# Performance work log

Hardware: AMD Instinct MI355X
Metric: run time of the kernel (lower is better)

## Reference

```python
import jax, jax.numpy as jnp
import numpy as np

N = 100000          # number of nodes (src == dst in this sampled graph)
DEG = 8             # uniform sampled fan-in (max_num_neighbors)
E = N * DEG         # number of edges
IN_C = 128
HEADS = 4
OUT_C = 32
NEG_SLOPE = 0.2


def setup_inputs() -> dict:
    key = jax.random.key(0)
    k1, k2, k3, k4, k5 = jax.random.split(key, 5)
    x = jax.random.normal(k1, (N, IN_C), dtype=jnp.float32)
    csr_row_ptr = jnp.arange(N + 1, dtype=jnp.int64) * DEG
    csr_col_ind = jax.random.randint(k2, (E,), 0, N, dtype=jnp.int64)
    # learned params (xavier-normal-ish scaling)
    lin_w = jax.random.normal(k3, (IN_C, HEADS * OUT_C), dtype=jnp.float32) * np.sqrt(2.0 / (IN_C + HEADS * OUT_C))
    att = jax.random.normal(k4, (2 * HEADS * OUT_C,), dtype=jnp.float32) * np.sqrt(2.0 / (1 + OUT_C))
    bias = jnp.zeros((HEADS * OUT_C,), dtype=jnp.float32)
    return {"x": x, "csr_row_ptr": csr_row_ptr, "csr_col_ind": csr_col_ind,
            "max_num_neighbors": DEG, "lin_w": lin_w, "att": att, "bias": bias}


def reference(x, csr_row_ptr, csr_col_ind, max_num_neighbors, lin_w, att, bias):
    n = x.shape[0]
    e = csr_col_ind.shape[0]
    hc = HEADS * OUT_C
    # linear projection: [N, H, C]
    xp = (x @ lin_w).reshape(n, HEADS, OUT_C)
    att_src = att[:hc].reshape(HEADS, OUT_C)
    att_dst = att[hc:].reshape(HEADS, OUT_C)
    # per-node attention logits per head: [N, H]
    a_src = jnp.einsum('nhc,hc->nh', xp, att_src)
    a_dst = jnp.einsum('nhc,hc->nh', xp, att_dst)
    # expand CSR row_ptr into per-edge destination ids: [E]
    dst = jnp.searchsorted(csr_row_ptr, jnp.arange(e, dtype=csr_row_ptr.dtype), side='right') - 1
    src = csr_col_ind
    # edge scores + per-destination softmax over incoming edges
    logits = jax.nn.leaky_relu(a_src[src] + a_dst[dst], NEG_SLOPE)  # [E, H]
    m = jax.ops.segment_max(logits, dst, num_segments=n)            # [N, H]
    ex = jnp.exp(logits - m[dst])
    denom = jax.ops.segment_sum(ex, dst, num_segments=n)            # [N, H]
    alpha = ex / denom[dst]                                         # [E, H]
    # weighted aggregation of neighbor features: [N, H, C]
    out = jax.ops.segment_sum(alpha[:, :, None] * xp[src], dst, num_segments=n)
    out = out.reshape(n, hc) + bias  # concat=True
    return out
```

## Files before the change

kernel.cpp:

```cpp
#include <hip/hip_runtime.h>
#include <stdint.h>

#define HEADS 4
#define NEG_SLOPE 0.2f
#define NPB 4
#define MB 128

typedef _Float16 f16;
typedef f16 f16x8 __attribute__((ext_vector_type(8)));
typedef f16 f16x2 __attribute__((ext_vector_type(2)));
typedef float f32x4 __attribute__((ext_vector_type(4)));

#define SWZ(row, kb) (((row) << 8) + ((kb) ^ (((row) & 7) << 4)))

__global__ __launch_bounds__(256) void wt_kernel(const float* __restrict__ w,
                                                 f16* __restrict__ wt) {
    __shared__ f16 tl[16][136];
    const int b = blockIdx.x, t = threadIdx.x;
    for (int i = t; i < 2048; i += 256) {
        int k = i >> 4, nl = i & 15;
        tl[nl][k] = (f16)w[k * 128 + b * 16 + nl];
    }
    __syncthreads();
    {
        int nl = t >> 4, kc = t & 15;
        f16x8 v = *(const f16x8*)&tl[nl][kc * 8];
        *(f16x8*)(wt + (b * 16 + nl) * 128 + kc * 8) = v;
    }
}

__global__ __launch_bounds__(256) void gat_proj_mfma(
    const float* __restrict__ x, const f16* __restrict__ wt,
    const float* __restrict__ att, f16* __restrict__ xp,
    float* __restrict__ a_src, float* __restrict__ a_dst, int n) {
    __shared__ unsigned char lds[65536];
    __shared__ float att_l[256];
    const int t = threadIdx.x;
    const int node0 = blockIdx.x * MB;
    const int lane = t & 63;
    const int wv = t >> 6;

    att_l[t] = att[t];

    for (int i = t; i < 2048; i += 256) {
        int row = i >> 4, kc = i & 15;
        uint4 v = *(const uint4*)(wt + row * 128 + kc * 8);
        *(uint4*)(lds + SWZ(row, kc * 16)) = v;
    }
    for (int i = t; i < 2048; i += 256) {
        int row = i >> 4, kc = i & 15;
        int grow = node0 + row;
        float4 a = make_float4(0.f, 0.f, 0.f, 0.f), b = a;
        if (grow < n) {
            const float4* p = (const float4*)(x + (size_t)grow * 128 + kc * 8);
            a = p[0];
            b = p[1];
        }
        f16x8 hv;
        hv[0] = (f16)a.x; hv[1] = (f16)a.y; hv[2] = (f16)a.z; hv[3] = (f16)a.w;
        hv[4] = (f16)b.x; hv[5] = (f16)b.y; hv[6] = (f16)b.z; hv[7] = (f16)b.w;
        *(f16x8*)(lds + 32768 + SWZ(row, kc * 16)) = hv;
    }
    __syncthreads();

    f32x4 acc[2][8];
#pragma unroll
    for (int mi = 0; mi < 2; mi++)
#pragma unroll
        for (int nf = 0; nf < 8; nf++)
            acc[mi][nf] = (f32x4){0.f, 0.f, 0.f, 0.f};

#pragma unroll
    for (int kt = 0; kt < 4; kt++) {
        const int kb = kt * 64 + (lane >> 4) * 16;
        f16x8 afr[2];
#pragma unroll
        for (int mi = 0; mi < 2; mi++) {
            int row = wv * 32 + mi * 16 + (lane & 15);
            afr[mi] = *(const f16x8*)(lds + 32768 + SWZ(row, kb));
        }
#pragma unroll
        for (int nf = 0; nf < 8; nf++) {
            int wrow = nf * 16 + (lane & 15);
            f16x8 bfr = *(const f16x8*)(lds + SWZ(wrow, kb));
            acc[0][nf] = __builtin_amdgcn_mfma_f32_16x16x32_f16(afr[0], bfr, acc[0][nf], 0, 0, 0);
            acc[1][nf] = __builtin_amdgcn_mfma_f32_16x16x32_f16(afr[1], bfr, acc[1][nf], 0, 0, 0);
        }
    }

    __syncthreads();
#pragma unroll
    for (int mi = 0; mi < 2; mi++)
#pragma unroll
        for (int r = 0; r < 4; r++) {
            int row = wv * 32 + mi * 16 + (lane >> 4) * 4 + r;
#pragma unroll
            for (int nf = 0; nf < 8; nf++) {
                int col = nf * 16 + (lane & 15);
                *(f16*)(lds + 32768 + SWZ(row, col * 2)) = (f16)acc[mi][nf][r];
            }
        }
    __syncthreads();

    for (int i = t; i < MB * HEADS; i += 256) {
        int row = i >> 2, h = i & 3;
        int grow = node0 + row;
        if (grow < n) {
            float s = 0.f, d = 0.f;
#pragma unroll
            for (int cc = 0; cc < 4; cc++) {
                f16x8 v = *(const f16x8*)(lds + 32768 + SWZ(row, h * 64 + cc * 16));
#pragma unroll
                for (int j = 0; j < 8; j++) {
                    float xv = (float)v[j];
                    int c = cc * 8 + j;
                    s = fmaf(xv, att_l[h * 32 + c], s);
                    d = fmaf(xv, att_l[128 + h * 32 + c], d);
                }
            }
            a_src[(size_t)grow * HEADS + h] = s;
            a_dst[(size_t)grow * HEADS + h] = d;
        }
    }
    for (int i = t; i < 2048; i += 256) {
        int row = i >> 4, kc = i & 15;
        int grow = node0 + row;
        if (grow < n)
            *(uint4*)(xp + (size_t)grow * 128 + kc * 8) =
                *(const uint4*)(lds + 32768 + SWZ(row, kc * 16));
    }
}

__global__ __launch_bounds__(256) void gat_aggr_kernel(
    const f16* __restrict__ xp, const float* __restrict__ a_src,
    const float* __restrict__ a_dst, const int* __restrict__ row_ptr,
    const int* __restrict__ col_ind, const float* __restrict__ bias,
    float* __restrict__ out, int n) {
    __shared__ float alpha_l[NPB][32];
    __shared__ int src_l[NPB][8];
    const int t = threadIdx.x;
    const int w = t >> 6;
    const int lane = t & 63;
    const int node = blockIdx.x * NPB + w;

    int deg = 0;
    if (node < n) {
        int rs = row_ptr[node];
        int re = row_ptr[node + 1];
        deg = re - rs;
        if (deg > 8) deg = 8;
        if (lane < 8) src_l[w][lane] = (lane < deg) ? col_ind[rs + lane] : 0;
    }
    __syncthreads();

    if (node < n && lane < 32) {
        const int e = lane >> 2, h = lane & 3;
        float v = -1e30f;
        if (e < deg) {
            int s = src_l[w][e];
            float z = a_src[(size_t)s * HEADS + h] + a_dst[(size_t)node * HEADS + h];
            v = (z >= 0.f) ? z : NEG_SLOPE * z;
        }
        float m = v;
        m = fmaxf(m, __shfl_xor(m, 4, 64));
        m = fmaxf(m, __shfl_xor(m, 8, 64));
        m = fmaxf(m, __shfl_xor(m, 16, 64));
        float ex = (e < deg) ? __expf(v - m) : 0.f;
        float ssum = ex;
        ssum += __shfl_xor(ssum, 4, 64);
        ssum += __shfl_xor(ssum, 8, 64);
        ssum += __shfl_xor(ssum, 16, 64);
        alpha_l[w][lane] = ex / ssum;
    }
    __syncthreads();
    if (node >= n) return;

    const int c0 = lane * 2;
    const int h = lane >> 4;
    float acc0 = 0.f, acc1 = 0.f;
    if (deg == 8) {
        f16x2 pv[8];
#pragma unroll
        for (int e = 0; e < 8; e++)
            pv[e] = *(const f16x2*)(xp + (size_t)src_l[w][e] * 128 + c0);
#pragma unroll
        for (int e = 0; e < 8; e++) {
            float a = alpha_l[w][e * 4 + h];
            acc0 = fmaf(a, (float)pv[e][0], acc0);
            acc1 = fmaf(a, (float)pv[e][1], acc1);
        }
    } else {
        for (int e = 0; e < deg; e++) {
            float a = alpha_l[w][e * 4 + h];
            f16x2 pv = *(const f16x2*)(xp + (size_t)src_l[w][e] * 128 + c0);
            acc0 = fmaf(a, (float)pv[0], acc0);
            acc1 = fmaf(a, (float)pv[1], acc1);
        }
    }
    float2 b2 = ((const float2*)bias)[lane];
    ((float2*)(out + (size_t)node * 128))[lane] = make_float2(acc0 + b2.x, acc1 + b2.y);
}

extern "C" void kernel_launch(void* const* d_in, const int* in_sizes, int n_in,
                              void* d_out, int out_size, void* d_ws, size_t ws_size,
                              hipStream_t stream) {
    const float* x = (const float*)d_in[0];
    const int* row_ptr = (const int*)d_in[1];
    const int* col_ind = (const int*)d_in[2];
    const float* lin_w = (const float*)d_in[4];
    const float* att = (const float*)d_in[5];
    const float* bias = (const float*)d_in[6];
    float* out = (float*)d_out;
    const int n = in_sizes[0] / 128;

    f16* xp = (f16*)d_ws;
    float* a_src = (float*)((char*)d_ws + (size_t)n * 128 * 2);
    float* a_dst = a_src + (size_t)n * HEADS;
    f16* wt = (f16*)(a_dst + (size_t)n * HEADS);

    hipLaunchKernelGGL(wt_kernel, dim3(8), dim3(256), 0, stream, lin_w, wt);
    hipLaunchKernelGGL(gat_proj_mfma, dim3((n + MB - 1) / MB), dim3(256), 0, stream,
                       x, wt, att, xp, a_src, a_dst, n);
    hipLaunchKernelGGL(gat_aggr_kernel, dim3((n + NPB - 1) / NPB), dim3(256), 0, stream,
                       xp, a_src, a_dst, row_ptr, col_ind, bias, out, n);
}
```

Before: 81.60 us.

## Shrink projection tile to 64 rows and make aggregation shared-memory-free

The projection kernel now handles 64 nodes per block with one 16-row MFMA tile per wave, which cuts LDS use and doubles the grid to raise occupancy. The aggregation kernel drops shared memory and block barriers. Source ids are broadcast with wave shuffles, the feature gathers are issued before the softmax so their latency is hidden, and each half-wave loads 8-byte f16x4 chunks for 4 edges before the halves are combined with a xor-shuffle. A zero-sum guard is added to the normalisation. The trade-off is extra shuffle work and idle upper lanes during the final store.

```diff
diff --git a/kernel.cpp b/kernel.cpp
--- a/kernel.cpp
+++ b/kernel.cpp
@@ -3,12 +3,11 @@
 
 #define HEADS 4
 #define NEG_SLOPE 0.2f
-#define NPB 4
-#define MB 128
+#define MB 64
 
 typedef _Float16 f16;
 typedef f16 f16x8 __attribute__((ext_vector_type(8)));
-typedef f16 f16x2 __attribute__((ext_vector_type(2)));
+typedef f16 f16x4 __attribute__((ext_vector_type(4)));
 typedef float f32x4 __attribute__((ext_vector_type(4)));
 
 #define SWZ(row, kb) (((row) << 8) + ((kb) ^ (((row) & 7) << 4)))
@@ -33,7 +32,7 @@
     const float* __restrict__ x, const f16* __restrict__ wt,
     const float* __restrict__ att, f16* __restrict__ xp,
     float* __restrict__ a_src, float* __restrict__ a_dst, int n) {
-    __shared__ unsigned char lds[65536];
+    __shared__ unsigned char lds[49152];
     __shared__ float att_l[256];
     const int t = threadIdx.x;
     const int node0 = blockIdx.x * MB;
@@ -47,7 +46,7 @@
         uint4 v = *(const uint4*)(wt + row * 128 + kc * 8);
         *(uint4*)(lds + SWZ(row, kc * 16)) = v;
     }
-    for (int i = t; i < 2048; i += 256) {
+    for (int i = t; i < 1024; i += 256) {
         int row = i >> 4, kc = i & 15;
         int grow = node0 + row;
         float4 a = make_float4(0.f, 0.f, 0.f, 0.f), b = a;
@@ -63,47 +62,37 @@
     }
     __syncthreads();
 
-    f32x4 acc[2][8];
-#pragma unroll
-    for (int mi = 0; mi < 2; mi++)
-#pragma unroll
-        for (int nf = 0; nf < 8; nf++)
-            acc[mi][nf] = (f32x4){0.f, 0.f, 0.f, 0.f};
+    f32x4 acc[8];
+#pragma unroll
+    for (int nf = 0; nf < 8; nf++) acc[nf] = (f32x4){0.f, 0.f, 0.f, 0.f};
 
 #pragma unroll
     for (int kt = 0; kt < 4; kt++) {
         const int kb = kt * 64 + (lane >> 4) * 16;
-        f16x8 afr[2];
-#pragma unroll
-        for (int mi = 0; mi < 2; mi++) {
-            int row = wv * 32 + mi * 16 + (lane & 15);
-            afr[mi] = *(const f16x8*)(lds + 32768 + SWZ(row, kb));
-        }
+        int arow = wv * 16 + (lane & 15);
+        f16x8 afr = *(const f16x8*)(lds + 32768 + SWZ(arow, kb));
 #pragma unroll
         for (int nf = 0; nf < 8; nf++) {
             int wrow = nf * 16 + (lane & 15);
             f16x8 bfr = *(const f16x8*)(lds + SWZ(wrow, kb));
-            acc[0][nf] = __builtin_amdgcn_mfma_f32_16x16x32_f16(afr[0], bfr, acc[0][nf], 0, 0, 0);
-            acc[1][nf] = __builtin_amdgcn_mfma_f32_16x16x32_f16(afr[1], bfr, acc[1][nf], 0, 0, 0);
-        }
-    }
-
-    __syncthreads();
-#pragma unroll
-    for (int mi = 0; mi < 2; mi++)
-#pragma unroll
-        for (int r = 0; r < 4; r++) {
-            int row = wv * 32 + mi * 16 + (lane >> 4) * 4 + r;
-#pragma unroll
-            for (int nf = 0; nf < 8; nf++) {
-                int col = nf * 16 + (lane & 15);
-                *(f16*)(lds + 32768 + SWZ(row, col * 2)) = (f16)acc[mi][nf][r];
-            }
-        }
-    __syncthreads();
-
-    for (int i = t; i < MB * HEADS; i += 256) {
-        int row = i >> 2, h = i & 3;
+            acc[nf] = __builtin_amdgcn_mfma_f32_16x16x32_f16(afr, bfr, acc[nf], 0, 0, 0);
+        }
+    }
+
+    __syncthreads();
+#pragma unroll
+    for (int r = 0; r < 4; r++) {
+        int row = wv * 16 + (lane >> 4) * 4 + r;
+#pragma unroll
+        for (int nf = 0; nf < 8; nf++) {
+            int col = nf * 16 + (lane & 15);
+            *(f16*)(lds + 32768 + SWZ(row, col * 2)) = (f16)acc[nf][r];
+        }
+    }
+    __syncthreads();
+
+    {
+        int row = t >> 2, h = t & 3;
         int grow = node0 + row;
         if (grow < n) {
             float s = 0.f, d = 0.f;
@@ -122,7 +111,7 @@
             a_dst[(size_t)grow * HEADS + h] = d;
         }
     }
-    for (int i = t; i < 2048; i += 256) {
+    for (int i = t; i < 1024; i += 256) {
         int row = i >> 4, kc = i & 15;
         int grow = node0 + row;
         if (grow < n)
@@ -136,69 +125,62 @@
     const float* __restrict__ a_dst, const int* __restrict__ row_ptr,
     const int* __restrict__ col_ind, const float* __restrict__ bias,
     float* __restrict__ out, int n) {
-    __shared__ float alpha_l[NPB][32];
-    __shared__ int src_l[NPB][8];
-    const int t = threadIdx.x;
-    const int w = t >> 6;
-    const int lane = t & 63;
-    const int node = blockIdx.x * NPB + w;
-
-    int deg = 0;
-    if (node < n) {
-        int rs = row_ptr[node];
-        int re = row_ptr[node + 1];
-        deg = re - rs;
-        if (deg > 8) deg = 8;
-        if (lane < 8) src_l[w][lane] = (lane < deg) ? col_ind[rs + lane] : 0;
-    }
-    __syncthreads();
-
-    if (node < n && lane < 32) {
-        const int e = lane >> 2, h = lane & 3;
-        float v = -1e30f;
-        if (e < deg) {
-            int s = src_l[w][e];
-            float z = a_src[(size_t)s * HEADS + h] + a_dst[(size_t)node * HEADS + h];
-            v = (z >= 0.f) ? z : NEG_SLOPE * z;
-        }
-        float m = v;
-        m = fmaxf(m, __shfl_xor(m, 4, 64));
-        m = fmaxf(m, __shfl_xor(m, 8, 64));
-        m = fmaxf(m, __shfl_xor(m, 16, 64));
-        float ex = (e < deg) ? __expf(v - m) : 0.f;
-        float ssum = ex;
-        ssum += __shfl_xor(ssum, 4, 64);
-        ssum += __shfl_xor(ssum, 8, 64);
-        ssum += __shfl_xor(ssum, 16, 64);
-        alpha_l[w][lane] = ex / ssum;
-    }
-    __syncthreads();
+    const int lane = threadIdx.x & 63;
+    const int node = blockIdx.x * 4 + (threadIdx.x >> 6);
     if (node >= n) return;
 
-    const int c0 = lane * 2;
-    const int h = lane >> 4;
-    float acc0 = 0.f, acc1 = 0.f;
-    if (deg == 8) {
-        f16x2 pv[8];
-#pragma unroll
-        for (int e = 0; e < 8; e++)
-            pv[e] = *(const f16x2*)(xp + (size_t)src_l[w][e] * 128 + c0);
-#pragma unroll
-        for (int e = 0; e < 8; e++) {
-            float a = alpha_l[w][e * 4 + h];
-            acc0 = fmaf(a, (float)pv[e][0], acc0);
-            acc1 = fmaf(a, (float)pv[e][1], acc1);
-        }
-    } else {
-        for (int e = 0; e < deg; e++) {
-            float a = alpha_l[w][e * 4 + h];
-            f16x2 pv = *(const f16x2*)(xp + (size_t)src_l[w][e] * 128 + c0);
-            acc0 = fmaf(a, (float)pv[0], acc0);
-            acc1 = fmaf(a, (float)pv[1], acc1);
-        }
-    }
-    float2 b2 = ((const float2*)bias)[lane];
-    ((float2*)(out + (size_t)node * 128))[lane] = make_float2(acc0 + b2.x, acc1 + b2.y);
+    int rs = row_ptr[node];
+    int deg = row_ptr[node + 1] - rs;
+    if (deg > 8) deg = 8;
+    int src0 = ((lane & 7) < deg) ? col_ind[rs + (lane & 7)] : 0;
+
+    const int p = lane >> 5, l = lane & 31;
+    f16x4 pv[4];
+#pragma unroll
+    for (int k = 0; k < 4; k++) {
+        int s = __shfl(src0, 2 * k + p, 64);
+        pv[k] = *(const f16x4*)(xp + (size_t)s * 128 + l * 4);
+    }
+
+    const int ea = (lane >> 2) & 7, ha = lane & 3;
+    int sa = __shfl(src0, ea, 64);
+    float v = -1e30f;
+    if (ea < deg) {
+        float z = a_src[(size_t)sa * HEADS + ha] + a_dst[(size_t)node * HEADS + ha];
+        v = (z >= 0.f) ? z : NEG_SLOPE * z;
+    }
+    float m = v;
+    m = fmaxf(m, __shfl_xor(m, 4, 64));
+    m = fmaxf(m, __shfl_xor(m, 8, 64));
+    m = fmaxf(m, __shfl_xor(m, 16, 64));
+    float ex = (ea < deg) ? __expf(v - m) : 0.f;
+    float ss = ex;
+    ss += __shfl_xor(ss, 4, 64);
+    ss += __shfl_xor(ss, 8, 64);
+    ss += __shfl_xor(ss, 16, 64);
+    float alpha = ex * ((ss > 0.f) ? (1.f / ss) : 0.f);
+
+    const int h = l >> 3;
+    float a0 = 0.f, a1 = 0.f, a2 = 0.f, a3 = 0.f;
+#pragma unroll
+    for (int k = 0; k < 4; k++) {
+        int e = 2 * k + p;
+        float a = __shfl(alpha, e * 4 + h, 32);
+        a0 = fmaf(a, (float)pv[k][0], a0);
+        a1 = fmaf(a, (float)pv[k][1], a1);
+        a2 = fmaf(a, (float)pv[k][2], a2);
+        a3 = fmaf(a, (float)pv[k][3], a3);
+    }
+    a0 += __shfl_xor(a0, 32, 64);
+    a1 += __shfl_xor(a1, 32, 64);
+    a2 += __shfl_xor(a2, 32, 64);
+    a3 += __shfl_xor(a3, 32, 64);
+
+    if (lane < 32) {
+        float4 b4 = ((const float4*)bias)[l];
+        float4 o = make_float4(a0 + b4.x, a1 + b4.y, a2 + b4.z, a3 + b4.w);
+        *(float4*)(out + (size_t)node * 128 + l * 4) = o;
+    }
 }
 
 extern "C" void kernel_launch(void* const* d_in, const int* in_sizes, int n_in,
@@ -221,6 +203,6 @@
     hipLaunchKernelGGL(wt_kernel, dim3(8), dim3(256), 0, stream, lin_w, wt);
     hipLaunchKernelGGL(gat_proj_mfma, dim3((n + MB - 1) / MB), dim3(256), 0, stream,
                        x, wt, att, xp, a_src, a_dst, n);
-    hipLaunchKernelGGL(gat_aggr_kernel, dim3((n + NPB - 1) / NPB), dim3(256), 0, stream,
+    hipLaunchKernelGGL(gat_aggr_kernel, dim3((n + 3) / 4), dim3(256), 0, stream,
                        xp, a_src, a_dst, row_ptr, col_ind, bias, out, n);
 }
```

New measurement: 76.62 us. -6.1%, faster.
